# Performance work log

Hardware: AMD Instinct MI355X
Metric: run time of the kernel (lower is better)

The kernel has to match this reference:

```python
import jax, jax.numpy as jnp
import numpy as np

N_NODES = 100000


def gcn_conv(x, W, b, src, dst, n):
    # PyG GCNConv: h = x @ W; add self-loops; sym-normalize; scatter-add to dst; + bias
    h = x @ W  # [N, out]
    loops = jnp.arange(n, dtype=src.dtype)
    src2 = jnp.concatenate([src, loops])
    dst2 = jnp.concatenate([dst, loops])
    deg = jax.ops.segment_sum(jnp.ones_like(dst2, dtype=h.dtype), dst2, num_segments=n)
    dinv = jnp.where(deg > 0, jax.lax.rsqrt(deg), 0.0)
    norm = dinv[src2] * dinv[dst2]  # [E+N]
    msg = h[src2] * norm[:, None]   # gather + scale
    out = jax.ops.segment_sum(msg, dst2, num_segments=n)  # scatter-add
    return out + b


def setup_inputs() -> dict:
    key = jax.random.key(0)
    k = jax.random.split(key, 6)
    N, F_IN, H, E = N_NODES, 128, 100, 3200000
    x = jax.random.normal(k[0], (N, F_IN), dtype=jnp.float32)
    edge_index = jax.random.randint(k[1], (2, E), 0, N, dtype=jnp.int64)
    W1 = jax.random.normal(k[2], (F_IN, H), dtype=jnp.float32) / np.sqrt(F_IN).astype(np.float32)
    b1 = jax.random.normal(k[3], (H,), dtype=jnp.float32) * 0.01
    W2 = jax.random.normal(k[4], (H, 1), dtype=jnp.float32) / np.sqrt(H).astype(np.float32)
    b2 = jax.random.normal(k[5], (1,), dtype=jnp.float32) * 0.01
    return {"x": x, "edge_index": edge_index, "W1": W1, "b1": b1, "W2": W2, "b2": b2}


def reference(x, edge_index, W1, b1, W2, b2) -> jnp.ndarray:
    src, dst = edge_index[0], edge_index[1]
    h = gcn_conv(x, W1, b1, src, dst, N_NODES)
    h = jax.nn.relu(h)
    out = gcn_conv(h, W2, b2, src, dst, N_NODES)  # [N, 1]
    return out
```

## Files before the change

### kernel.cpp

```cpp
#include <hip/hip_runtime.h>

#define F_IN 128
#define H1 100
#define G1LD 128
#define CAP 80
#define CH_A 4096
#define SCAN_BLK 256
#define SCAN_CH 1024
#define NBIN_MAX 256

__device__ __forceinline__ float bf2f(unsigned short v) {
    union { unsigned u; float f; } x;
    x.u = ((unsigned)v) << 16;
    return x.f;
}
__device__ __forceinline__ unsigned short f2bf(float f) {
    union { float f; unsigned u; } x;
    x.f = f;
    unsigned u = x.u;
    u += 0x7FFF + ((u >> 16) & 1);
    return (unsigned short)(u >> 16);
}
__device__ __forceinline__ float bflo(unsigned v) {
    union { unsigned u; float f; } x;
    x.u = v << 16;
    return x.f;
}
__device__ __forceinline__ float bfhi(unsigned v) {
    union { unsigned u; float f; } x;
    x.u = v & 0xFFFF0000u;
    return x.f;
}

__global__ __launch_bounds__(256) void k_histA(const int* __restrict__ dst, int* __restrict__ M,
                                               int E, int n, int nbin, int nbA) {
    __shared__ int hist[NBIN_MAX];
    const int tid = threadIdx.x;
    hist[tid] = 0;
    __syncthreads();
    const int base = blockIdx.x * CH_A;
    const int lim = min(CH_A, E - base);
    for (int j = tid; j < lim; j += 256) {
        unsigned d = (unsigned)dst[base + j];
        if (d >= (unsigned)n) d = 0;
        atomicAdd(&hist[d >> 9], 1);
    }
    __syncthreads();
    for (int b = tid; b < nbin; b += 256) M[b * nbA + blockIdx.x] = hist[b];
}

__global__ __launch_bounds__(SCAN_BLK) void k_blocksums(const int* __restrict__ v,
                                                        int* __restrict__ bsum, int m) {
    __shared__ int sd[SCAN_BLK];
    const int tid = threadIdx.x;
    const int base = blockIdx.x * SCAN_CH + tid * 4;
    int s = 0;
    #pragma unroll
    for (int j = 0; j < 4; ++j) {
        int i = base + j;
        if (i < m) s += v[i];
    }
    sd[tid] = s;
    __syncthreads();
    for (int off = SCAN_BLK / 2; off > 0; off >>= 1) {
        if (tid < off) sd[tid] += sd[tid + off];
        __syncthreads();
    }
    if (tid == 0) bsum[blockIdx.x] = sd[0];
}

__global__ __launch_bounds__(256) void k_scan_bsums(int* __restrict__ bsum, int nb) {
    __shared__ int sd[256];
    const int tid = threadIdx.x;
    const int v = (tid < nb) ? bsum[tid] : 0;
    sd[tid] = v;
    __syncthreads();
    for (int off = 1; off < 256; off <<= 1) {
        int t = (tid >= off) ? sd[tid - off] : 0;
        __syncthreads();
        sd[tid] += t;
        __syncthreads();
    }
    if (tid < nb) bsum[tid] = sd[tid] - v;
}

__global__ __launch_bounds__(SCAN_BLK) void k_scan_write(const int* __restrict__ v,
                                                         const int* __restrict__ bsum,
                                                         int* __restrict__ out, int m) {
    __shared__ int sd[SCAN_BLK];
    const int tid = threadIdx.x;
    const int base = blockIdx.x * SCAN_CH + tid * 4;
    int c[4];
    int s = 0;
    #pragma unroll
    for (int j = 0; j < 4; ++j) {
        int i = base + j;
        c[j] = (i < m) ? v[i] : 0;
        s += c[j];
    }
    const int own = s;
    sd[tid] = s;
    __syncthreads();
    for (int off = 1; off < SCAN_BLK; off <<= 1) {
        int t = (tid >= off) ? sd[tid - off] : 0;
        __syncthreads();
        sd[tid] += t;
        __syncthreads();
    }
    int pre = sd[tid] - own + bsum[blockIdx.x];
    #pragma unroll
    for (int j = 0; j < 4; ++j) {
        int i = base + j;
        if (i < m) {
            out[i] = pre;
            pre += c[j];
        }
    }
}

__global__ __launch_bounds__(256) void k_binC(const int* __restrict__ src, const int* __restrict__ dst,
                                              const int* __restrict__ Mscan, unsigned* __restrict__ pk,
                                              int E, int n, int nbin, int nbA) {
    __shared__ int hist[NBIN_MAX];
    __shared__ int loff[NBIN_MAX];
    const int tid = threadIdx.x;
    hist[tid] = 0;
    for (int b = tid; b < nbin; b += 256) loff[b] = Mscan[b * nbA + blockIdx.x];
    __syncthreads();
    const int base = blockIdx.x * CH_A;
    const int lim = min(CH_A, E - base);
    for (int j = tid; j < lim; j += 256) {
        unsigned d = (unsigned)dst[base + j];
        unsigned s = (unsigned)src[base + j];
        if (d >= (unsigned)n) d = 0;
        if (s >= (unsigned)n) s = 0;
        const int bin = d >> 9;
        const int r = atomicAdd(&hist[bin], 1);
        pk[loff[bin] + r] = (s << 9) | (d & 511u);
    }
}

__global__ __launch_bounds__(256) void k_binD(const unsigned* __restrict__ pk,
                                              const int* __restrict__ Mscan,
                                              int* __restrict__ ebuf, int* __restrict__ counts,
                                              int E, int n, int nbin, int nbA) {
    __shared__ int fcnt[512];
    const int tid = threadIdx.x;
    fcnt[tid] = 0;
    fcnt[tid + 256] = 0;
    __syncthreads();
    const int b = blockIdx.x;
    const int bstart = Mscan[b * nbA];
    const int bend = (b + 1 < nbin) ? Mscan[(b + 1) * nbA] : E;
    for (int j = bstart + tid; j < bend; j += 256) {
        const unsigned v = pk[j];
        const int dlow = (int)(v & 511u);
        const int s = (int)(v >> 9);
        const int r = atomicAdd(&fcnt[dlow], 1);
        if (r < CAP) ebuf[((b << 9) + dlow) * CAP + r] = s;
    }
    __syncthreads();
    for (int t = tid; t < 512; t += 256) {
        const int d = (b << 9) + t;
        if (d < n) counts[d] = fcnt[t];
    }
}

__global__ __launch_bounds__(128) void k_gemm1(
    const float* __restrict__ x, const float* __restrict__ W1,
    const int* __restrict__ counts, unsigned short* __restrict__ g, int n) {
    __shared__ float xs[8][F_IN];
    const int f = threadIdx.x;
    const int nb = blockIdx.x * 8;

    {
        const float4* xv = (const float4*)(x + (long)nb * F_IN);
        float4* xsv = (float4*)&xs[0][0];
        #pragma unroll
        for (int i = threadIdx.x; i < 256; i += 128) {
            int node = nb + (i >> 5);
            xsv[i] = (node < n) ? xv[i] : make_float4(0.f, 0.f, 0.f, 0.f);
        }
    }
    __syncthreads();

    const bool act = (f < H1);
    float accv[8] = {0, 0, 0, 0, 0, 0, 0, 0};

    for (int kc = 0; kc < F_IN; kc += 8) {
        float w[8];
        #pragma unroll
        for (int j = 0; j < 8; ++j) w[j] = act ? W1[(kc + j) * H1 + f] : 0.0f;
        #pragma unroll
        for (int v = 0; v < 8; ++v) {
            const float4 b0 = *(const float4*)&xs[v][kc];
            const float4 b1 = *(const float4*)&xs[v][kc + 4];
            float s = accv[v];
            s = fmaf(b0.x, w[0], s);
            s = fmaf(b0.y, w[1], s);
            s = fmaf(b0.z, w[2], s);
            s = fmaf(b0.w, w[3], s);
            s = fmaf(b1.x, w[4], s);
            s = fmaf(b1.y, w[5], s);
            s = fmaf(b1.z, w[6], s);
            s = fmaf(b1.w, w[7], s);
            accv[v] = s;
        }
    }

    if (act) {
        #pragma unroll
        for (int v = 0; v < 8; ++v) {
            int node = nb + v;
            if (node < n) {
                float di = rsqrtf(1.0f + (float)counts[node]);
                g[(node << 7) + f] = f2bf(accv[v] * di);
            }
        }
    }
}

__global__ __launch_bounds__(256) void k_agg1(
    const unsigned short* __restrict__ g1, const int* __restrict__ counts,
    const int* __restrict__ ebuf,
    const float* __restrict__ b1, const float* __restrict__ W2,
    float* __restrict__ g2, int n) {
    const int lane = threadIdx.x & 63;
    const int node = blockIdx.x * 4 + (threadIdx.x >> 6);
    if (node >= n) return;

    const int c = counts[node];
    const int cnt = (c < CAP) ? c : CAP;
    const int* __restrict__ eb = ebuf + node * CAP;
    const unsigned* __restrict__ gp = (const unsigned*)g1;
    const bool act = (lane < H1 / 2);

    const unsigned v0 = gp[(node << 6) + lane];
    float pa0 = bflo(v0), pa1 = 0.f, pa2 = 0.f, pa3 = 0.f;
    float pb0 = bfhi(v0), pb1 = 0.f, pb2 = 0.f, pb3 = 0.f;

    int j = 0;
    for (; j + 8 <= cnt; j += 8) {
        const int u0 = eb[j] << 6;
        const int u1 = eb[j + 1] << 6;
        const int u2 = eb[j + 2] << 6;
        const int u3 = eb[j + 3] << 6;
        const int u4 = eb[j + 4] << 6;
        const int u5 = eb[j + 5] << 6;
        const int u6 = eb[j + 6] << 6;
        const int u7 = eb[j + 7] << 6;
        const unsigned w0 = gp[u0 + lane];
        const unsigned w1 = gp[u1 + lane];
        const unsigned w2 = gp[u2 + lane];
        const unsigned w3 = gp[u3 + lane];
        const unsigned w4 = gp[u4 + lane];
        const unsigned w5 = gp[u5 + lane];
        const unsigned w6 = gp[u6 + lane];
        const unsigned w7 = gp[u7 + lane];
        pa0 += bflo(w0); pb0 += bfhi(w0);
        pa1 += bflo(w1); pb1 += bfhi(w1);
        pa2 += bflo(w2); pb2 += bfhi(w2);
        pa3 += bflo(w3); pb3 += bfhi(w3);
        pa0 += bflo(w4); pb0 += bfhi(w4);
        pa1 += bflo(w5); pb1 += bfhi(w5);
        pa2 += bflo(w6); pb2 += bfhi(w6);
        pa3 += bflo(w7); pb3 += bfhi(w7);
    }
    for (; j < cnt; ++j) {
        const unsigned w = gp[(eb[j] << 6) + lane];
        pa0 += bflo(w);
        pb0 += bfhi(w);
    }

    const float di = rsqrtf(1.0f + (float)c);
    float sum = 0.f;
    if (act) {
        const float sa = (pa0 + pa1) + (pa2 + pa3);
        const float sb = (pb0 + pb1) + (pb2 + pb3);
        const float2 bb = ((const float2*)b1)[lane];
        const float2 ww = ((const float2*)W2)[lane];
        sum = fmaxf(fmaf(di, sa, bb.x), 0.f) * ww.x + fmaxf(fmaf(di, sb, bb.y), 0.f) * ww.y;
    }
    #pragma unroll
    for (int off = 32; off > 0; off >>= 1) sum += __shfl_down(sum, off);
    if (lane == 0) g2[node] = di * sum;
}

__global__ __launch_bounds__(256) void k_agg2(
    const float* __restrict__ g2, const int* __restrict__ counts,
    const int* __restrict__ ebuf, const float* __restrict__ b2,
    float* __restrict__ out, int n) {
    const int lane = threadIdx.x & 63;
    const int node = blockIdx.x * 4 + (threadIdx.x >> 6);
    if (node >= n) return;
    const int c = counts[node];
    const int cnt = (c < CAP) ? c : CAP;
    const int* __restrict__ eb = ebuf + node * CAP;
    float s = 0.f;
    for (int j = lane; j < cnt; j += 64) s += g2[eb[j]];
    #pragma unroll
    for (int off = 32; off > 0; off >>= 1) s += __shfl_down(s, off);
    if (lane == 0) {
        float di = rsqrtf(1.0f + (float)c);
        out[node] = fmaf(di, g2[node] + s, b2[0]);
    }
}

extern "C" void kernel_launch(void* const* d_in, const int* in_sizes, int n_in,
                              void* d_out, int out_size, void* d_ws, size_t ws_size,
                              hipStream_t stream) {
    const float* x  = (const float*)d_in[0];
    const int*   ei = (const int*)d_in[1];
    const float* W1 = (const float*)d_in[2];
    const float* b1 = (const float*)d_in[3];
    const float* W2 = (const float*)d_in[4];
    const float* b2 = (const float*)d_in[5];

    const int n = in_sizes[0] / F_IN;
    const int E = in_sizes[1] / 2;
    const int* src = ei;
    const int* dst = ei + E;

    const int nbin = (n + 511) >> 9;
    const int nbA  = (E + CH_A - 1) / CH_A;
    const int m    = nbin * nbA;
    const int nbScan = (m + SCAN_CH - 1) / SCAN_CH;

    char* p = (char*)d_ws;
    int* counts = (int*)p;                   p += (size_t)n * 4;
    float* g2   = (float*)p;                 p += (size_t)n * 4;
    p = (char*)(((size_t)p + 255) & ~(size_t)255);
    unsigned short* g1 = (unsigned short*)p; p += (size_t)n * G1LD * 2;
    int* ebuf   = (int*)p;                   p += (size_t)n * CAP * 4;
    unsigned* pk = (unsigned*)p;             p += (size_t)E * 4;
    int* M      = (int*)p;                   p += (size_t)m * 4;
    int* Mscan  = (int*)p;                   p += (size_t)m * 4;
    int* bsum   = (int*)p;                   p += 1024;
    float* out = (float*)d_out;

    k_histA<<<nbA, 256, 0, stream>>>(dst, M, E, n, nbin, nbA);
    k_blocksums<<<nbScan, SCAN_BLK, 0, stream>>>(M, bsum, m);
    k_scan_bsums<<<1, 256, 0, stream>>>(bsum, nbScan);
    k_scan_write<<<nbScan, SCAN_BLK, 0, stream>>>(M, bsum, Mscan, m);
    k_binC<<<nbA, 256, 0, stream>>>(src, dst, Mscan, pk, E, n, nbin, nbA);
    k_binD<<<nbin, 256, 0, stream>>>(pk, Mscan, ebuf, counts, E, n, nbin, nbA);
    k_gemm1<<<(n + 7) / 8, 128, 0, stream>>>(x, W1, counts, g1, n);
    k_agg1<<<(n + 3) / 4, 256, 0, stream>>>(g1, counts, ebuf, b1, W2, g2, n);
    k_agg2<<<(n + 3) / 4, 256, 0, stream>>>(g2, counts, ebuf, b2, out, n);
}
```

Baseline: 381.6 us.

## Restructure bin scan, pad edge lists to 16, widen gemm1 and binD blocks

Replaces the three-kernel global scan with a per-bin row scan plus a small bin-base scan, removing one launch. binD now uses 512 threads and pads each node's edge list up to a multiple of 16 with a sentinel index pointing at a zeroed extra row of g1. This lets agg1 read indices as int4 and run a branch-free 16-way unrolled gather with no scalar tail, at the cost of some wasted gathers of the zero row. gemm1 now processes 16 nodes per block to reuse W1 loads and also writes the zero sentinel row.

Result: faster. 357.5 us (-6.3%).

```diff
diff --git a/kernel.cpp b/kernel.cpp
--- a/kernel.cpp
+++ b/kernel.cpp
@@ -5,15 +5,8 @@
 #define G1LD 128
 #define CAP 80
 #define CH_A 4096
-#define SCAN_BLK 256
-#define SCAN_CH 1024
 #define NBIN_MAX 256
 
-__device__ __forceinline__ float bf2f(unsigned short v) {
-    union { unsigned u; float f; } x;
-    x.u = ((unsigned)v) << 16;
-    return x.f;
-}
 __device__ __forceinline__ unsigned short f2bf(float f) {
     union { float f; unsigned u; } x;
     x.f = f;
@@ -49,31 +42,23 @@
     for (int b = tid; b < nbin; b += 256) M[b * nbA + blockIdx.x] = hist[b];
 }
 
-__global__ __launch_bounds__(SCAN_BLK) void k_blocksums(const int* __restrict__ v,
-                                                        int* __restrict__ bsum, int m) {
-    __shared__ int sd[SCAN_BLK];
-    const int tid = threadIdx.x;
-    const int base = blockIdx.x * SCAN_CH + tid * 4;
+__global__ __launch_bounds__(256) void k_scanRows(const int* __restrict__ M,
+                                                  int* __restrict__ Mscan,
+                                                  int* __restrict__ T, int nbA) {
+    __shared__ int sd[256];
+    const int tid = threadIdx.x;
+    const int b = blockIdx.x;
+    const int base = tid * 4;
+    int c[4];
     int s = 0;
     #pragma unroll
     for (int j = 0; j < 4; ++j) {
         int i = base + j;
-        if (i < m) s += v[i];
-    }
+        c[j] = (i < nbA) ? M[b * nbA + i] : 0;
+        s += c[j];
+    }
+    const int own = s;
     sd[tid] = s;
-    __syncthreads();
-    for (int off = SCAN_BLK / 2; off > 0; off >>= 1) {
-        if (tid < off) sd[tid] += sd[tid + off];
-        __syncthreads();
-    }
-    if (tid == 0) bsum[blockIdx.x] = sd[0];
-}
-
-__global__ __launch_bounds__(256) void k_scan_bsums(int* __restrict__ bsum, int nb) {
-    __shared__ int sd[256];
-    const int tid = threadIdx.x;
-    const int v = (tid < nb) ? bsum[tid] : 0;
-    sd[tid] = v;
     __syncthreads();
     for (int off = 1; off < 256; off <<= 1) {
         int t = (tid >= off) ? sd[tid - off] : 0;
@@ -81,51 +66,42 @@
         sd[tid] += t;
         __syncthreads();
     }
-    if (tid < nb) bsum[tid] = sd[tid] - v;
-}
-
-__global__ __launch_bounds__(SCAN_BLK) void k_scan_write(const int* __restrict__ v,
-                                                         const int* __restrict__ bsum,
-                                                         int* __restrict__ out, int m) {
-    __shared__ int sd[SCAN_BLK];
-    const int tid = threadIdx.x;
-    const int base = blockIdx.x * SCAN_CH + tid * 4;
-    int c[4];
-    int s = 0;
+    int pre = sd[tid] - own;
     #pragma unroll
     for (int j = 0; j < 4; ++j) {
         int i = base + j;
-        c[j] = (i < m) ? v[i] : 0;
-        s += c[j];
-    }
-    const int own = s;
-    sd[tid] = s;
-    __syncthreads();
-    for (int off = 1; off < SCAN_BLK; off <<= 1) {
+        if (i < nbA) {
+            Mscan[b * nbA + i] = pre;
+            pre += c[j];
+        }
+    }
+    if (tid == 255) T[b] = sd[255];
+}
+
+__global__ __launch_bounds__(256) void k_scanBins(const int* __restrict__ T,
+                                                  int* __restrict__ binBase, int nbin) {
+    __shared__ int sd[256];
+    const int tid = threadIdx.x;
+    const int v = (tid < nbin) ? T[tid] : 0;
+    sd[tid] = v;
+    __syncthreads();
+    for (int off = 1; off < 256; off <<= 1) {
         int t = (tid >= off) ? sd[tid - off] : 0;
         __syncthreads();
         sd[tid] += t;
         __syncthreads();
     }
-    int pre = sd[tid] - own + bsum[blockIdx.x];
-    #pragma unroll
-    for (int j = 0; j < 4; ++j) {
-        int i = base + j;
-        if (i < m) {
-            out[i] = pre;
-            pre += c[j];
-        }
-    }
+    if (tid < nbin) binBase[tid] = sd[tid] - v;
 }
 
 __global__ __launch_bounds__(256) void k_binC(const int* __restrict__ src, const int* __restrict__ dst,
-                                              const int* __restrict__ Mscan, unsigned* __restrict__ pk,
-                                              int E, int n, int nbin, int nbA) {
+                                              const int* __restrict__ Mscan, const int* __restrict__ binBase,
+                                              unsigned* __restrict__ pk, int E, int n, int nbin, int nbA) {
     __shared__ int hist[NBIN_MAX];
     __shared__ int loff[NBIN_MAX];
     const int tid = threadIdx.x;
     hist[tid] = 0;
-    for (int b = tid; b < nbin; b += 256) loff[b] = Mscan[b * nbA + blockIdx.x];
+    for (int b = tid; b < nbin; b += 256) loff[b] = binBase[b] + Mscan[b * nbA + blockIdx.x];
     __syncthreads();
     const int base = blockIdx.x * CH_A;
     const int lim = min(CH_A, E - base);
@@ -140,19 +116,18 @@
     }
 }
 
-__global__ __launch_bounds__(256) void k_binD(const unsigned* __restrict__ pk,
-                                              const int* __restrict__ Mscan,
+__global__ __launch_bounds__(512) void k_binD(const unsigned* __restrict__ pk,
+                                              const int* __restrict__ binBase,
                                               int* __restrict__ ebuf, int* __restrict__ counts,
-                                              int E, int n, int nbin, int nbA) {
+                                              int E, int n, int nbin) {
     __shared__ int fcnt[512];
     const int tid = threadIdx.x;
     fcnt[tid] = 0;
-    fcnt[tid + 256] = 0;
     __syncthreads();
     const int b = blockIdx.x;
-    const int bstart = Mscan[b * nbA];
-    const int bend = (b + 1 < nbin) ? Mscan[(b + 1) * nbA] : E;
-    for (int j = bstart + tid; j < bend; j += 256) {
+    const int bstart = binBase[b];
+    const int bend = (b + 1 < nbin) ? binBase[b + 1] : E;
+    for (int j = bstart + tid; j < bend; j += 512) {
         const unsigned v = pk[j];
         const int dlow = (int)(v & 511u);
         const int s = (int)(v >> 9);
@@ -160,39 +135,46 @@
         if (r < CAP) ebuf[((b << 9) + dlow) * CAP + r] = s;
     }
     __syncthreads();
-    for (int t = tid; t < 512; t += 256) {
-        const int d = (b << 9) + t;
-        if (d < n) counts[d] = fcnt[t];
+    const int d = (b << 9) + tid;
+    if (d < n) {
+        const int c = min(fcnt[tid], CAP);
+        counts[d] = fcnt[tid];
+        const int cp = min((c + 15) & ~15, CAP);
+        int* __restrict__ row = ebuf + d * CAP;
+        for (int r = c; r < cp; ++r) row[r] = n;
     }
 }
 
 __global__ __launch_bounds__(128) void k_gemm1(
     const float* __restrict__ x, const float* __restrict__ W1,
     const int* __restrict__ counts, unsigned short* __restrict__ g, int n) {
-    __shared__ float xs[8][F_IN];
+    __shared__ float xs[16][F_IN];
     const int f = threadIdx.x;
-    const int nb = blockIdx.x * 8;
+    const int nb = blockIdx.x * 16;
 
     {
         const float4* xv = (const float4*)(x + (long)nb * F_IN);
         float4* xsv = (float4*)&xs[0][0];
         #pragma unroll
-        for (int i = threadIdx.x; i < 256; i += 128) {
-            int node = nb + (i >> 5);
+        for (int k = 0; k < 4; ++k) {
+            const int i = f + k * 128;
+            const int node = nb + (i >> 5);
             xsv[i] = (node < n) ? xv[i] : make_float4(0.f, 0.f, 0.f, 0.f);
         }
     }
     __syncthreads();
 
     const bool act = (f < H1);
-    float accv[8] = {0, 0, 0, 0, 0, 0, 0, 0};
+    float accv[16];
+    #pragma unroll
+    for (int v = 0; v < 16; ++v) accv[v] = 0.f;
 
     for (int kc = 0; kc < F_IN; kc += 8) {
         float w[8];
         #pragma unroll
         for (int j = 0; j < 8; ++j) w[j] = act ? W1[(kc + j) * H1 + f] : 0.0f;
         #pragma unroll
-        for (int v = 0; v < 8; ++v) {
+        for (int v = 0; v < 16; ++v) {
             const float4 b0 = *(const float4*)&xs[v][kc];
             const float4 b1 = *(const float4*)&xs[v][kc + 4];
             float s = accv[v];
@@ -210,11 +192,13 @@
 
     if (act) {
         #pragma unroll
-        for (int v = 0; v < 8; ++v) {
-            int node = nb + v;
+        for (int v = 0; v < 16; ++v) {
+            const int node = nb + v;
             if (node < n) {
-                float di = rsqrtf(1.0f + (float)counts[node]);
+                const float di = rsqrtf(1.0f + (float)counts[node]);
                 g[(node << 7) + f] = f2bf(accv[v] * di);
+            } else if (node == n) {
+                g[(node << 7) + f] = 0;
             }
         }
     }
@@ -231,32 +215,35 @@
 
     const int c = counts[node];
     const int cnt = (c < CAP) ? c : CAP;
-    const int* __restrict__ eb = ebuf + node * CAP;
+    const int cntp = min((cnt + 15) & ~15, CAP);
+    const int4* __restrict__ ebq = (const int4*)(ebuf + node * CAP);
     const unsigned* __restrict__ gp = (const unsigned*)g1;
-    const bool act = (lane < H1 / 2);
 
     const unsigned v0 = gp[(node << 6) + lane];
     float pa0 = bflo(v0), pa1 = 0.f, pa2 = 0.f, pa3 = 0.f;
     float pb0 = bfhi(v0), pb1 = 0.f, pb2 = 0.f, pb3 = 0.f;
 
-    int j = 0;
-    for (; j + 8 <= cnt; j += 8) {
-        const int u0 = eb[j] << 6;
-        const int u1 = eb[j + 1] << 6;
-        const int u2 = eb[j + 2] << 6;
-        const int u3 = eb[j + 3] << 6;
-        const int u4 = eb[j + 4] << 6;
-        const int u5 = eb[j + 5] << 6;
-        const int u6 = eb[j + 6] << 6;
-        const int u7 = eb[j + 7] << 6;
-        const unsigned w0 = gp[u0 + lane];
-        const unsigned w1 = gp[u1 + lane];
-        const unsigned w2 = gp[u2 + lane];
-        const unsigned w3 = gp[u3 + lane];
-        const unsigned w4 = gp[u4 + lane];
-        const unsigned w5 = gp[u5 + lane];
-        const unsigned w6 = gp[u6 + lane];
-        const unsigned w7 = gp[u7 + lane];
+    for (int j = 0; j < cntp; j += 16) {
+        const int4 e0 = ebq[(j >> 2)];
+        const int4 e1 = ebq[(j >> 2) + 1];
+        const int4 e2 = ebq[(j >> 2) + 2];
+        const int4 e3 = ebq[(j >> 2) + 3];
+        const unsigned w0 = gp[(e0.x << 6) + lane];
+        const unsigned w1 = gp[(e0.y << 6) + lane];
+        const unsigned w2 = gp[(e0.z << 6) + lane];
+        const unsigned w3 = gp[(e0.w << 6) + lane];
+        const unsigned w4 = gp[(e1.x << 6) + lane];
+        const unsigned w5 = gp[(e1.y << 6) + lane];
+        const unsigned w6 = gp[(e1.z << 6) + lane];
+        const unsigned w7 = gp[(e1.w << 6) + lane];
+        const unsigned w8 = gp[(e2.x << 6) + lane];
+        const unsigned w9 = gp[(e2.y << 6) + lane];
+        const unsigned wa = gp[(e2.z << 6) + lane];
+        const unsigned wb = gp[(e2.w << 6) + lane];
+        const unsigned wc = gp[(e3.x << 6) + lane];
+        const unsigned wd = gp[(e3.y << 6) + lane];
+        const unsigned we = gp[(e3.z << 6) + lane];
+        const unsigned wf = gp[(e3.w << 6) + lane];
         pa0 += bflo(w0); pb0 += bfhi(w0);
         pa1 += bflo(w1); pb1 += bfhi(w1);
         pa2 += bflo(w2); pb2 += bfhi(w2);
@@ -265,16 +252,19 @@
         pa1 += bflo(w5); pb1 += bfhi(w5);
         pa2 += bflo(w6); pb2 += bfhi(w6);
         pa3 += bflo(w7); pb3 += bfhi(w7);
-    }
-    for (; j < cnt; ++j) {
-        const unsigned w = gp[(eb[j] << 6) + lane];
-        pa0 += bflo(w);
-        pb0 += bfhi(w);
+        pa0 += bflo(w8); pb0 += bfhi(w8);
+        pa1 += bflo(w9); pb1 += bfhi(w9);
+        pa2 += bflo(wa); pb2 += bfhi(wa);
+        pa3 += bflo(wb); pb3 += bfhi(wb);
+        pa0 += bflo(wc); pb0 += bfhi(wc);
+        pa1 += bflo(wd); pb1 += bfhi(wd);
+        pa2 += bflo(we); pb2 += bfhi(we);
+        pa3 += bflo(wf); pb3 += bfhi(wf);
     }
 
     const float di = rsqrtf(1.0f + (float)c);
     float sum = 0.f;
-    if (act) {
+    if (lane < H1 / 2) {
         const float sa = (pa0 + pa1) + (pa2 + pa3);
         const float sb = (pb0 + pb1) + (pb2 + pb3);
         const float2 bb = ((const float2*)b1)[lane];
@@ -324,27 +314,27 @@
     const int nbin = (n + 511) >> 9;
     const int nbA  = (E + CH_A - 1) / CH_A;
     const int m    = nbin * nbA;
-    const int nbScan = (m + SCAN_CH - 1) / SCAN_CH;
 
     char* p = (char*)d_ws;
     int* counts = (int*)p;                   p += (size_t)n * 4;
     float* g2   = (float*)p;                 p += (size_t)n * 4;
     p = (char*)(((size_t)p + 255) & ~(size_t)255);
-    unsigned short* g1 = (unsigned short*)p; p += (size_t)n * G1LD * 2;
+    unsigned short* g1 = (unsigned short*)p; p += (size_t)(n + 1) * G1LD * 2;
+    p = (char*)(((size_t)p + 255) & ~(size_t)255);
     int* ebuf   = (int*)p;                   p += (size_t)n * CAP * 4;
     unsigned* pk = (unsigned*)p;             p += (size_t)E * 4;
     int* M      = (int*)p;                   p += (size_t)m * 4;
     int* Mscan  = (int*)p;                   p += (size_t)m * 4;
-    int* bsum   = (int*)p;                   p += 1024;
+    int* T      = (int*)p;                   p += 1024;
+    int* binBase = (int*)p;                  p += 1024;
     float* out = (float*)d_out;
 
     k_histA<<<nbA, 256, 0, stream>>>(dst, M, E, n, nbin, nbA);
-    k_blocksums<<<nbScan, SCAN_BLK, 0, stream>>>(M, bsum, m);
-    k_scan_bsums<<<1, 256, 0, stream>>>(bsum, nbScan);
-    k_scan_write<<<nbScan, SCAN_BLK, 0, stream>>>(M, bsum, Mscan, m);
-    k_binC<<<nbA, 256, 0, stream>>>(src, dst, Mscan, pk, E, n, nbin, nbA);
-    k_binD<<<nbin, 256, 0, stream>>>(pk, Mscan, ebuf, counts, E, n, nbin, nbA);
-    k_gemm1<<<(n + 7) / 8, 128, 0, stream>>>(x, W1, counts, g1, n);
+    k_scanRows<<<nbin, 256, 0, stream>>>(M, Mscan, T, nbA);
+    k_scanBins<<<1, 256, 0, stream>>>(T, binBase, nbin);
+    k_binC<<<nbA, 256, 0, stream>>>(src, dst, Mscan, binBase, pk, E, n, nbin, nbA);
+    k_binD<<<nbin, 512, 0, stream>>>(pk, binBase, ebuf, counts, E, n, nbin);
+    k_gemm1<<<(n + 16) / 16, 128, 0, stream>>>(x, W1, counts, g1, n);
     k_agg1<<<(n + 3) / 4, 256, 0, stream>>>(g1, counts, ebuf, b1, W2, g2, n);
     k_agg2<<<(n + 3) / 4, 256, 0, stream>>>(g2, counts, ebuf, b2, out, n);
 }
```
